# Optimization experiments

Measured on AMD Instinct MI355X. Metric: run time of the kernel, lower is better.

## Reference

```python
import jax, jax.numpy as jnp
import numpy as np

D_MODEL = 1024
N_HEADS = 16
D_HEAD = D_MODEL // N_HEADS
B, T = 4, 2048


def setup_inputs() -> dict:
    key = jax.random.key(0)
    k1, k2, k3 = jax.random.split(key, 3)
    x = jax.random.normal(k1, (B, T, D_MODEL), dtype=jnp.float32)
    # match nn.Linear init scale roughly (uniform ~ 1/sqrt(fan_in)); scale normal for stability
    w_qkv = jax.random.normal(k2, (D_MODEL, 3 * D_MODEL), dtype=jnp.float32) / np.sqrt(D_MODEL)
    w_out = jax.random.normal(k3, (D_MODEL, D_MODEL), dtype=jnp.float32) / np.sqrt(D_MODEL)
    return {"x": x, "w_qkv": w_qkv, "w_out": w_out}


def reference(x, w_qkv, w_out):
    Bx, Tx, D = x.shape
    H, Dh = N_HEADS, D_HEAD
    qkv = x @ w_qkv                                  # [B,T,3D]
    qkv = qkv.reshape(Bx, Tx, 3, H, Dh)
    q, k, v = qkv[:, :, 0], qkv[:, :, 1], qkv[:, :, 2]  # [B,T,H,Dh]
    scores = jnp.einsum('bqhd,bkhd->bhqk', q, k) / np.sqrt(Dh).astype(np.float32)
    mask = jnp.triu(jnp.ones((Tx, Tx), dtype=bool), k=1)  # causal: mask future
    scores = jnp.where(mask, -jnp.inf, scores)
    attn = jax.nn.softmax(scores, axis=-1)
    out = jnp.einsum('bhqk,bkhd->bqhd', attn, v).reshape(Bx, Tx, D)
    return out @ w_out
```

## Files before the change

kernel.cpp:

```cpp
#include <hip/hip_runtime.h>
#include <math.h>

#define T_SEQ 2048
#define NB 4
#define NH 16
#define DH 64
#define DM 1024

typedef __attribute__((ext_vector_type(8))) __bf16 bf16x8;
typedef __attribute__((ext_vector_type(4))) float f32x4;

typedef const __attribute__((address_space(1))) void* gas_t;
typedef __attribute__((address_space(3))) void* las_t;

__device__ inline bool detect_f32(const unsigned short* probe, int lane) {
    unsigned short u = probe[lane];
    int e = (u >> 7) & 0xFF;
    bool outlier = (e >= 140) || (e <= 90 && (u & 0x7fff) != 0);
    unsigned long long m = __ballot(outlier);
    return __popcll(m) >= 4;
}

__device__ inline bf16x8 load8_flex(const void* base, long elem, bool f32) {
    if (!f32) {
        return *(const bf16x8*)((const __bf16*)base + elem);
    } else {
        const float* f = (const float*)base + elem;
        float4 a = *(const float4*)f;
        float4 b = *(const float4*)(f + 4);
        bf16x8 r;
        r[0] = (__bf16)a.x; r[1] = (__bf16)a.y; r[2] = (__bf16)a.z; r[3] = (__bf16)a.w;
        r[4] = (__bf16)b.x; r[5] = (__bf16)b.y; r[6] = (__bf16)b.z; r[7] = (__bf16)b.w;
        return r;
    }
}

__global__ __launch_bounds__(256)
void cvt_x(const float* __restrict__ in, __bf16* __restrict__ out, long n8) {
    long i = (long)blockIdx.x * blockDim.x + threadIdx.x;
    if (i >= n8) return;
    const float* f = in + i * 8;
    float4 a = *(const float4*)f;
    float4 b = *(const float4*)(f + 4);
    bf16x8 r;
    r[0] = (__bf16)a.x; r[1] = (__bf16)a.y; r[2] = (__bf16)a.z; r[3] = (__bf16)a.w;
    r[4] = (__bf16)b.x; r[5] = (__bf16)b.y; r[6] = (__bf16)b.z; r[7] = (__bf16)b.w;
    *(bf16x8*)(out + i * 8) = r;
}

__global__ __launch_bounds__(256)
void tpose_cvt(const float* __restrict__ in, __bf16* __restrict__ out, int R, int C) {
    __shared__ __bf16 tile[32][33];
    const int bx = blockIdx.x * 32;
    const int by = blockIdx.y * 32;
    const int tx = threadIdx.x & 31;
    const int ty = threadIdx.x >> 5;
#pragma unroll
    for (int it = 0; it < 4; ++it) {
        int r = ty + it * 8;
        tile[r][tx] = (__bf16)in[(long)(by + r) * C + bx + tx];
    }
    __syncthreads();
#pragma unroll
    for (int it = 0; it < 4; ++it) {
        int r = ty + it * 8;
        out[(long)(bx + r) * R + by + tx] = tile[tx][r];
    }
}

__global__ __launch_bounds__(256)
void gemm_bt(const __bf16* __restrict__ A, long lda,
             const __bf16* __restrict__ Bt, long ldb,
             void* __restrict__ C, long ldc, int c_f32, int K) {
    __shared__ __align__(16) __bf16 sA[128 * 32];
    __shared__ __align__(16) __bf16 sB[128 * 32];
    const int tid  = threadIdx.x;
    const int lane = tid & 63;
    const int wave = tid >> 6;
    const int l15  = lane & 15;
    const int quad = lane >> 4;
    const int bm = blockIdx.y * 128;
    const int bn = blockIdx.x * 128;
    const int wm = (wave & 1) * 64;
    const int wn = (wave >> 1) * 64;

    f32x4 zero = {0.f, 0.f, 0.f, 0.f};
    f32x4 acc[4][4];
#pragma unroll
    for (int i = 0; i < 4; ++i)
#pragma unroll
        for (int j = 0; j < 4; ++j) acc[i][j] = zero;

    const int srow = tid >> 2;
    const int scol = (tid & 3) * 8;
    const __bf16* gA0 = A  + (long)(bm + srow) * lda + scol;
    const __bf16* gA1 = A  + (long)(bm + 64 + srow) * lda + scol;
    const __bf16* gB0 = Bt + (long)(bn + srow) * ldb + scol;
    const __bf16* gB1 = Bt + (long)(bn + 64 + srow) * ldb + scol;

    __bf16* lA0 = sA + wave * 512;
    __bf16* lA1 = sA + 2048 + wave * 512;
    __bf16* lB0 = sB + wave * 512;
    __bf16* lB1 = sB + 2048 + wave * 512;

    for (int k0 = 0; k0 < K; k0 += 32) {
        __syncthreads();
        __builtin_amdgcn_global_load_lds((gas_t)(gA0 + k0), (las_t)lA0, 16, 0, 0);
        __builtin_amdgcn_global_load_lds((gas_t)(gA1 + k0), (las_t)lA1, 16, 0, 0);
        __builtin_amdgcn_global_load_lds((gas_t)(gB0 + k0), (las_t)lB0, 16, 0, 0);
        __builtin_amdgcn_global_load_lds((gas_t)(gB1 + k0), (las_t)lB1, 16, 0, 0);
        __syncthreads();

        bf16x8 af[4], bfm[4];
#pragma unroll
        for (int i = 0; i < 4; ++i)
            af[i] = *(const bf16x8*)(sA + (wm + i * 16 + l15) * 32 + quad * 8);
#pragma unroll
        for (int j = 0; j < 4; ++j)
            bfm[j] = *(const bf16x8*)(sB + (wn + j * 16 + l15) * 32 + quad * 8);
#pragma unroll
        for (int i = 0; i < 4; ++i)
#pragma unroll
            for (int j = 0; j < 4; ++j)
                acc[i][j] = __builtin_amdgcn_mfma_f32_16x16x32_bf16(af[i], bfm[j], acc[i][j], 0, 0, 0);
    }

#pragma unroll
    for (int i = 0; i < 4; ++i)
#pragma unroll
        for (int j = 0; j < 4; ++j)
#pragma unroll
            for (int r = 0; r < 4; ++r) {
                int row = bm + wm + i * 16 + quad * 4 + r;
                int col = bn + wn + j * 16 + l15;
                if (c_f32)
                    ((float*)C)[(long)row * ldc + col] = acc[i][j][r];
                else
                    ((__bf16*)C)[(long)row * ldc + col] = (__bf16)acc[i][j][r];
            }
}

__global__ __launch_bounds__(256)
void gemm_bn(const void* __restrict__ A, long lda, long a0, int a_flex,
             const void* __restrict__ B, long ldb, int b_flex,
             void* __restrict__ C, long ldc, int c_flex, int K,
             const unsigned short* __restrict__ probe) {
    __shared__ __align__(16) __bf16 sA[128 * 32];
    __shared__ __align__(16) __bf16 sB[128 * 32];
    const int tid  = threadIdx.x;
    const int lane = tid & 63;
    const int wave = tid >> 6;
    const int l15  = lane & 15;
    const int quad = lane >> 4;
    const int bm = blockIdx.y * 128;
    const int bn = blockIdx.x * 128;
    const int wm = (wave & 1) * 64;
    const int wn = (wave >> 1) * 64;

    const bool is_f32 = detect_f32(probe, lane);
    const bool a_f32 = a_flex && is_f32;
    const bool b_f32 = b_flex && is_f32;
    const bool c_f32 = c_flex && is_f32;

    f32x4 zero = {0.f, 0.f, 0.f, 0.f};
    f32x4 acc[4][4];
#pragma unroll
    for (int i = 0; i < 4; ++i)
#pragma unroll
        for (int j = 0; j < 4; ++j) acc[i][j] = zero;

    const int srow = tid >> 2;
    const int scol = (tid & 3) * 8;

    for (int k0 = 0; k0 < K; k0 += 32) {
        __syncthreads();
        *(bf16x8*)(sA + tid * 8) =
            load8_flex(A, a0 + (long)(bm + srow) * lda + k0 + scol, a_f32);
        *(bf16x8*)(sA + 2048 + tid * 8) =
            load8_flex(A, a0 + (long)(bm + 64 + srow) * lda + k0 + scol, a_f32);
#pragma unroll
        for (int it = 0; it < 2; ++it) {
            int idx = tid + it * 256;
            int kk  = idx & 31;
            int n8  = (idx >> 5) * 8;
            bf16x8 bv = load8_flex(B, (long)(k0 + kk) * ldb + bn + n8, b_f32);
#pragma unroll
            for (int jj = 0; jj < 8; ++jj) sB[(n8 + jj) * 32 + kk] = bv[jj];
        }
        __syncthreads();

        bf16x8 af[4], bfm[4];
#pragma unroll
        for (int i = 0; i < 4; ++i)
            af[i] = *(const bf16x8*)(sA + (wm + i * 16 + l15) * 32 + quad * 8);
#pragma unroll
        for (int j = 0; j < 4; ++j)
            bfm[j] = *(const bf16x8*)(sB + (wn + j * 16 + l15) * 32 + quad * 8);
#pragma unroll
        for (int i = 0; i < 4; ++i)
#pragma unroll
            for (int j = 0; j < 4; ++j)
                acc[i][j] = __builtin_amdgcn_mfma_f32_16x16x32_bf16(af[i], bfm[j], acc[i][j], 0, 0, 0);
    }

#pragma unroll
    for (int i = 0; i < 4; ++i)
#pragma unroll
        for (int j = 0; j < 4; ++j)
#pragma unroll
            for (int r = 0; r < 4; ++r) {
                int row = bm + wm + i * 16 + quad * 4 + r;
                int col = bn + wn + j * 16 + l15;
                if (c_f32)
                    ((float*)C)[(long)row * ldc + col] = acc[i][j][r];
                else
                    ((__bf16*)C)[(long)row * ldc + col] = (__bf16)acc[i][j][r];
            }
}

__global__ __launch_bounds__(256)
void attn_k(__bf16* __restrict__ qkvp, int bhbits) {
    const int bid  = blockIdx.x;
    const int qt   = bid >> bhbits;
    const int bh   = bid & ((1 << bhbits) - 1);
    const int h    = bh & 15;
    const int b    = bh >> 4;
    const int tid  = threadIdx.x;
    const int lane = tid & 63;
    const int wave = tid >> 6;
    const int l15  = lane & 15;
    const int quad = lane >> 4;

    __shared__ __align__(16) __bf16 sK[64 * 72];
    __shared__ __align__(16) __bf16 sVT[64 * 64];
    __shared__ __align__(16) __bf16 sP[4][32 * 64];

    const long rs = 3 * DM;
    __bf16* base = qkvp + (long)b * T_SEQ * rs + h * DH;

    const int sr  = tid >> 3;
    const int sm  = tid & 7;
    const int sc8 = sm * 8;
    const int rot = 8 * ((5 * sm) & 7);
    const int vc0 = (sr + rot) & 63;
    const int vc1 = (sr + 32 + rot) & 63;

    const int q0  = qt * 128;
    const int wq0 = q0 + wave * 32;

    bf16x8 qa[2][2];
#pragma unroll
    for (int i = 0; i < 2; ++i)
#pragma unroll
        for (int kk = 0; kk < 2; ++kk) {
            bf16x8 v = *(const bf16x8*)(base + (long)(wq0 + i * 16 + l15) * rs + kk * 32 + quad * 8);
#pragma unroll
            for (int jj = 0; jj < 8; ++jj) v[jj] = (__bf16)((float)v[jj] * 0.125f);
            qa[i][kk] = v;
        }

    f32x4 zero = {0.f, 0.f, 0.f, 0.f};
    f32x4 o[2][4], o4[2];
#pragma unroll
    for (int i = 0; i < 2; ++i) {
        o4[i] = zero;
#pragma unroll
        for (int j = 0; j < 4; ++j) o[i][j] = zero;
    }

    bf16x8 vone;
#pragma unroll
    for (int jj = 0; jj < 8; ++jj) vone[jj] = (__bf16)1.0f;

    const int nk = (q0 + 128) >> 6;

    bf16x8 kreg[2], vreg[2];
#pragma unroll
    for (int it = 0; it < 2; ++it) {
        const __bf16* rp = base + (long)(sr + it * 32) * rs;
        kreg[it] = *(const bf16x8*)(rp + DM + sc8);
        vreg[it] = *(const bf16x8*)(rp + 2 * DM + sc8);
    }

    for (int t = 0; t < nk; ++t) {
        const int k0 = t * 64;
        __syncthreads();
        *(bf16x8*)(sK + sr * 72 + sc8)        = kreg[0];
        *(bf16x8*)(sK + (sr + 32) * 72 + sc8) = kreg[1];
#pragma unroll
        for (int jj = 0; jj < 8; ++jj) {
            sVT[(sc8 + jj) * 64 + vc0] = vreg[0][jj];
            sVT[(sc8 + jj) * 64 + vc1] = vreg[1][jj];
        }
        __syncthreads();

        if (t + 1 < nk) {
#pragma unroll
            for (int it = 0; it < 2; ++it) {
                const __bf16* rp = base + (long)(k0 + 64 + sr + it * 32) * rs;
                kreg[it] = *(const bf16x8*)(rp + DM + sc8);
                vreg[it] = *(const bf16x8*)(rp + 2 * DM + sc8);
            }
        }

        const bool active = (k0 <= wq0 + 31);
        if (active) {
            f32x4 s[2][4];
#pragma unroll
            for (int i = 0; i < 2; ++i)
#pragma unroll
                for (int j = 0; j < 4; ++j) s[i][j] = zero;
#pragma unroll
            for (int kk = 0; kk < 2; ++kk) {
                bf16x8 kb[4];
#pragma unroll
                for (int j = 0; j < 4; ++j)
                    kb[j] = *(const bf16x8*)(sK + (j * 16 + l15) * 72 + kk * 32 + quad * 8);
#pragma unroll
                for (int i = 0; i < 2; ++i)
#pragma unroll
                    for (int j = 0; j < 4; ++j)
                        s[i][j] = __builtin_amdgcn_mfma_f32_16x16x32_bf16(qa[i][kk], kb[j], s[i][j], 0, 0, 0);
            }

            const bool needmask = (k0 + 63 > wq0);
#pragma unroll
            for (int i = 0; i < 2; ++i)
#pragma unroll
                for (int r = 0; r < 4; ++r) {
                    const int qg = wq0 + i * 16 + quad * 4 + r;
#pragma unroll
                    for (int j = 0; j < 4; ++j) {
                        const int kg = k0 + j * 16 + l15;
                        float pv = __expf(fminf(s[i][j][r], 60.f));
                        if (needmask) pv = (kg > qg) ? 0.f : pv;
                        sP[wave][(i * 16 + quad * 4 + r) * 64 +
                                 ((j * 16 + l15 + 16 * quad) & 63)] = (__bf16)pv;
                    }
                }
        }

        __builtin_amdgcn_sched_barrier(0);
        __builtin_amdgcn_s_waitcnt(0xc07f);
        __builtin_amdgcn_sched_barrier(0);

        if (active) {
#pragma unroll
            for (int kk = 0; kk < 2; ++kk) {
                bf16x8 pa[2], vb[4];
#pragma unroll
                for (int i = 0; i < 2; ++i)
                    pa[i] = *(const bf16x8*)(
                        &sP[wave][(i * 16 + l15) * 64 +
                                  ((kk * 32 + quad * 8 + 16 * (l15 >> 2)) & 63)]);
#pragma unroll
                for (int j = 0; j < 4; ++j) {
                    const int g = (2 * j + (l15 >> 3)) & 7;
                    vb[j] = *(const bf16x8*)(
                        sVT + (j * 16 + l15) * 64 +
                        ((kk * 32 + quad * 8 + 8 * ((5 * g) & 7)) & 63));
                }
#pragma unroll
                for (int i = 0; i < 2; ++i) {
#pragma unroll
                    for (int j = 0; j < 4; ++j)
                        o[i][j] = __builtin_amdgcn_mfma_f32_16x16x32_bf16(pa[i], vb[j], o[i][j], 0, 0, 0);
                    o4[i] = __builtin_amdgcn_mfma_f32_16x16x32_bf16(pa[i], vone, o4[i], 0, 0, 0);
                }
            }
        }
    }

#pragma unroll
    for (int i = 0; i < 2; ++i)
#pragma unroll
        for (int r = 0; r < 4; ++r) {
            const int qg  = wq0 + i * 16 + quad * 4 + r;
            const float inv = 1.f / o4[i][r];
#pragma unroll
            for (int j = 0; j < 4; ++j)
                base[(long)qg * rs + j * 16 + l15] = (__bf16)(o[i][j][r] * inv);
        }
}

__global__ __launch_bounds__(256)
void fallback_k(float* __restrict__ out, long n, float wsmb) {
    long i = (long)blockIdx.x * blockDim.x + threadIdx.x;
    for (; i < n; i += (long)gridDim.x * blockDim.x) out[i] = 0.f;
    if (blockIdx.x == 0 && threadIdx.x == 0) out[0] = wsmb;
}

extern "C" void kernel_launch(void* const* d_in, const int* in_sizes, int n_in,
                              void* d_out, int out_size, void* d_ws, size_t ws_size,
                              hipStream_t stream) {
    const void* x     = d_in[0];
    const void* w_qkv = d_in[1];
    const void* w_out = d_in[2];
    const unsigned short* probe = (const unsigned short*)d_in[0];

    __bf16* qkv = (__bf16*)d_ws;
    __bf16* xb  = qkv + (size_t)8192 * 3072;
    __bf16* wtq = xb  + (size_t)8192 * 1024;
    __bf16* wto = wtq + (size_t)3072 * 1024;

    const size_t NEED_T1   = (size_t)72 * 1024 * 1024;
    const size_t NEED_FULL = (size_t)8192 * 3072 * 2;
    const size_t NEED_B    = (size_t)2048 * 3072 * 2;

    if (ws_size >= NEED_T1) {
        cvt_x<<<dim3(4096), 256, 0, stream>>>((const float*)x, xb, (long)8192 * 1024 / 8);
        tpose_cvt<<<dim3(96, 32), 256, 0, stream>>>((const float*)w_qkv, wtq, 1024, 3072);
        tpose_cvt<<<dim3(32, 32), 256, 0, stream>>>((const float*)w_out, wto, 1024, 1024);
        gemm_bt<<<dim3(24, 64), 256, 0, stream>>>(xb, 1024, wtq, 1024, qkv, 3072, 0, 1024);
        attn_k<<<dim3(16 * 64), 256, 0, stream>>>(qkv, 6);
        gemm_bt<<<dim3(8, 64), 256, 0, stream>>>(qkv, 3072, wto, 1024, d_out, 1024, 1, 1024);
    } else if (ws_size >= NEED_FULL) {
        gemm_bn<<<dim3(24, 64), 256, 0, stream>>>(
            x, 1024, 0, 1, w_qkv, 3072, 1, qkv, 3072, 0, 1024, probe);
        attn_k<<<dim3(16 * 64), 256, 0, stream>>>(qkv, 6);
        gemm_bn<<<dim3(8, 64), 256, 0, stream>>>(
            qkv, 3072, 0, 0, w_out, 1024, 1, d_out, 1024, 1, 1024, probe);
    } else if (ws_size >= NEED_B) {
        for (int b = 0; b < NB; ++b) {
            long xoff = (long)b * T_SEQ * DM;
            gemm_bn<<<dim3(24, 16), 256, 0, stream>>>(
                x, 1024, xoff, 1, w_qkv, 3072, 1, qkv, 3072, 0, 1024, probe);
            attn_k<<<dim3(16 * 16), 256, 0, stream>>>(qkv, 4);
            gemm_bn<<<dim3(8, 16), 256, 0, stream>>>(
                qkv, 3072, 0, 0, w_out, 1024, 1,
                (void*)((char*)d_out + (size_t)b * T_SEQ * DM * 4),
                1024, 1, 1024, probe);
        }
    } else {
        fallback_k<<<dim3(512), 256, 0, stream>>>(
            (float*)d_out, (long)8192 * 1024, (float)(ws_size >> 20));
    }
}
```

Baseline: 307.7 us.

## Pair causal query tiles per block and use 8 waves of 16 rows

The attention kernel now launches 512-thread blocks with 8 waves, each wave owning 16 query rows instead of 32. Each block processes two query tiles (p and 15-p) in sequence, which balances the causal workload across blocks and halves the grid. Each K/V tile staged into shared memory is shared by more waves, and fewer registers are needed per wave. The cost is less MFMA reuse of each K/V fragment per wave and a serialized second pass inside every block.

```diff
diff --git a/kernel.cpp b/kernel.cpp
--- a/kernel.cpp
+++ b/kernel.cpp
@@ -218,10 +218,10 @@
             }
 }
 
-__global__ __launch_bounds__(256)
+__global__ __launch_bounds__(512, 4)
 void attn_k(__bf16* __restrict__ qkvp, int bhbits) {
     const int bid  = blockIdx.x;
-    const int qt   = bid >> bhbits;
+    const int p    = bid >> bhbits;
     const int bh   = bid & ((1 << bhbits) - 1);
     const int h    = bh & 15;
     const int b    = bh >> 4;
@@ -233,7 +233,7 @@
 
     __shared__ __align__(16) __bf16 sK[64 * 72];
     __shared__ __align__(16) __bf16 sVT[64 * 64];
-    __shared__ __align__(16) __bf16 sP[4][32 * 64];
+    __shared__ __align__(16) __bf16 sP[8][16 * 64];
 
     const long rs = 3 * DM;
     __bf16* base = qkvp + (long)b * T_SEQ * rs + h * DH;
@@ -242,145 +242,123 @@
     const int sm  = tid & 7;
     const int sc8 = sm * 8;
     const int rot = 8 * ((5 * sm) & 7);
-    const int vc0 = (sr + rot) & 63;
-    const int vc1 = (sr + 32 + rot) & 63;
-
-    const int q0  = qt * 128;
-    const int wq0 = q0 + wave * 32;
-
-    bf16x8 qa[2][2];
-#pragma unroll
-    for (int i = 0; i < 2; ++i)
+    const int vcol = (sr + rot) & 63;
+
+    bf16x8 vone;
+#pragma unroll
+    for (int jj = 0; jj < 8; ++jj) vone[jj] = (__bf16)1.0f;
+
+    f32x4 zero = {0.f, 0.f, 0.f, 0.f};
+
+#pragma unroll 1
+    for (int half = 0; half < 2; ++half) {
+        const int qt  = half ? (15 - p) : p;
+        const int q0  = qt * 128;
+        const int wq0 = q0 + wave * 16;
+        const int nk  = (q0 + 128) >> 6;
+
+        bf16x8 qa[2];
 #pragma unroll
         for (int kk = 0; kk < 2; ++kk) {
-            bf16x8 v = *(const bf16x8*)(base + (long)(wq0 + i * 16 + l15) * rs + kk * 32 + quad * 8);
+            bf16x8 v = *(const bf16x8*)(base + (long)(wq0 + l15) * rs + kk * 32 + quad * 8);
 #pragma unroll
             for (int jj = 0; jj < 8; ++jj) v[jj] = (__bf16)((float)v[jj] * 0.125f);
-            qa[i][kk] = v;
-        }
-
-    f32x4 zero = {0.f, 0.f, 0.f, 0.f};
-    f32x4 o[2][4], o4[2];
-#pragma unroll
-    for (int i = 0; i < 2; ++i) {
-        o4[i] = zero;
-#pragma unroll
-        for (int j = 0; j < 4; ++j) o[i][j] = zero;
-    }
-
-    bf16x8 vone;
-#pragma unroll
-    for (int jj = 0; jj < 8; ++jj) vone[jj] = (__bf16)1.0f;
-
-    const int nk = (q0 + 128) >> 6;
-
-    bf16x8 kreg[2], vreg[2];
-#pragma unroll
-    for (int it = 0; it < 2; ++it) {
-        const __bf16* rp = base + (long)(sr + it * 32) * rs;
-        kreg[it] = *(const bf16x8*)(rp + DM + sc8);
-        vreg[it] = *(const bf16x8*)(rp + 2 * DM + sc8);
-    }
-
-    for (int t = 0; t < nk; ++t) {
-        const int k0 = t * 64;
-        __syncthreads();
-        *(bf16x8*)(sK + sr * 72 + sc8)        = kreg[0];
-        *(bf16x8*)(sK + (sr + 32) * 72 + sc8) = kreg[1];
-#pragma unroll
-        for (int jj = 0; jj < 8; ++jj) {
-            sVT[(sc8 + jj) * 64 + vc0] = vreg[0][jj];
-            sVT[(sc8 + jj) * 64 + vc1] = vreg[1][jj];
-        }
-        __syncthreads();
-
-        if (t + 1 < nk) {
-#pragma unroll
-            for (int it = 0; it < 2; ++it) {
-                const __bf16* rp = base + (long)(k0 + 64 + sr + it * 32) * rs;
-                kreg[it] = *(const bf16x8*)(rp + DM + sc8);
-                vreg[it] = *(const bf16x8*)(rp + 2 * DM + sc8);
+            qa[kk] = v;
+        }
+
+        f32x4 o[4], o4;
+        o4 = zero;
+#pragma unroll
+        for (int j = 0; j < 4; ++j) o[j] = zero;
+
+        bf16x8 kreg, vreg;
+        {
+            const __bf16* rp = base + (long)sr * rs;
+            kreg = *(const bf16x8*)(rp + DM + sc8);
+            vreg = *(const bf16x8*)(rp + 2 * DM + sc8);
+        }
+
+        for (int t = 0; t < nk; ++t) {
+            const int k0 = t * 64;
+            __syncthreads();
+            *(bf16x8*)(sK + sr * 72 + sc8) = kreg;
+#pragma unroll
+            for (int jj = 0; jj < 8; ++jj)
+                sVT[(sc8 + jj) * 64 + vcol] = vreg[jj];
+            __syncthreads();
+
+            if (t + 1 < nk) {
+                const __bf16* rp = base + (long)(k0 + 64 + sr) * rs;
+                kreg = *(const bf16x8*)(rp + DM + sc8);
+                vreg = *(const bf16x8*)(rp + 2 * DM + sc8);
             }
-        }
-
-        const bool active = (k0 <= wq0 + 31);
-        if (active) {
-            f32x4 s[2][4];
-#pragma unroll
-            for (int i = 0; i < 2; ++i)
-#pragma unroll
-                for (int j = 0; j < 4; ++j) s[i][j] = zero;
-#pragma unroll
-            for (int kk = 0; kk < 2; ++kk) {
-                bf16x8 kb[4];
-#pragma unroll
-                for (int j = 0; j < 4; ++j)
-                    kb[j] = *(const bf16x8*)(sK + (j * 16 + l15) * 72 + kk * 32 + quad * 8);
-#pragma unroll
-                for (int i = 0; i < 2; ++i)
+
+            const bool active = (k0 <= wq0 + 15);
+            if (active) {
+                f32x4 s[4];
+#pragma unroll
+                for (int j = 0; j < 4; ++j) s[j] = zero;
+#pragma unroll
+                for (int kk = 0; kk < 2; ++kk) {
+                    bf16x8 kb[4];
 #pragma unroll
                     for (int j = 0; j < 4; ++j)
-                        s[i][j] = __builtin_amdgcn_mfma_f32_16x16x32_bf16(qa[i][kk], kb[j], s[i][j], 0, 0, 0);
-            }
-
-            const bool needmask = (k0 + 63 > wq0);
-#pragma unroll
-            for (int i = 0; i < 2; ++i)
+                        kb[j] = *(const bf16x8*)(sK + (j * 16 + l15) * 72 + kk * 32 + quad * 8);
+#pragma unroll
+                    for (int j = 0; j < 4; ++j)
+                        s[j] = __builtin_amdgcn_mfma_f32_16x16x32_bf16(qa[kk], kb[j], s[j], 0, 0, 0);
+                }
+
+                const bool needmask = (k0 + 63 > wq0);
 #pragma unroll
                 for (int r = 0; r < 4; ++r) {
-                    const int qg = wq0 + i * 16 + quad * 4 + r;
+                    const int qg = wq0 + quad * 4 + r;
 #pragma unroll
                     for (int j = 0; j < 4; ++j) {
                         const int kg = k0 + j * 16 + l15;
-                        float pv = __expf(fminf(s[i][j][r], 60.f));
+                        float pv = __expf(fminf(s[j][r], 60.f));
                         if (needmask) pv = (kg > qg) ? 0.f : pv;
-                        sP[wave][(i * 16 + quad * 4 + r) * 64 +
+                        sP[wave][(quad * 4 + r) * 64 +
                                  ((j * 16 + l15 + 16 * quad) & 63)] = (__bf16)pv;
                     }
                 }
-        }
-
-        __builtin_amdgcn_sched_barrier(0);
-        __builtin_amdgcn_s_waitcnt(0xc07f);
-        __builtin_amdgcn_sched_barrier(0);
-
-        if (active) {
-#pragma unroll
-            for (int kk = 0; kk < 2; ++kk) {
-                bf16x8 pa[2], vb[4];
-#pragma unroll
-                for (int i = 0; i < 2; ++i)
-                    pa[i] = *(const bf16x8*)(
-                        &sP[wave][(i * 16 + l15) * 64 +
+            }
+
+            __builtin_amdgcn_sched_barrier(0);
+            __builtin_amdgcn_s_waitcnt(0xc07f);
+            __builtin_amdgcn_sched_barrier(0);
+
+            if (active) {
+#pragma unroll
+                for (int kk = 0; kk < 2; ++kk) {
+                    bf16x8 pa, vb[4];
+                    pa = *(const bf16x8*)(
+                        &sP[wave][l15 * 64 +
                                   ((kk * 32 + quad * 8 + 16 * (l15 >> 2)) & 63)]);
 #pragma unroll
-                for (int j = 0; j < 4; ++j) {
-                    const int g = (2 * j + (l15 >> 3)) & 7;
-                    vb[j] = *(const bf16x8*)(
-                        sVT + (j * 16 + l15) * 64 +
-                        ((kk * 32 + quad * 8 + 8 * ((5 * g) & 7)) & 63));
-                }
-#pragma unroll
-                for (int i = 0; i < 2; ++i) {
+                    for (int j = 0; j < 4; ++j) {
+                        const int g = (2 * j + (l15 >> 3)) & 7;
+                        vb[j] = *(const bf16x8*)(
+                            sVT + (j * 16 + l15) * 64 +
+                            ((kk * 32 + quad * 8 + 8 * ((5 * g) & 7)) & 63));
+                    }
 #pragma unroll
                     for (int j = 0; j < 4; ++j)
-                        o[i][j] = __builtin_amdgcn_mfma_f32_16x16x32_bf16(pa[i], vb[j], o[i][j], 0, 0, 0);
-                    o4[i] = __builtin_amdgcn_mfma_f32_16x16x32_bf16(pa[i], vone, o4[i], 0, 0, 0);
+                        o[j] = __builtin_amdgcn_mfma_f32_16x16x32_bf16(pa, vb[j], o[j], 0, 0, 0);
+                    o4 = __builtin_amdgcn_mfma_f32_16x16x32_bf16(pa, vone, o4, 0, 0, 0);
                 }
             }
         }
-    }
-
-#pragma unroll
-    for (int i = 0; i < 2; ++i)
+
 #pragma unroll
         for (int r = 0; r < 4; ++r) {
-            const int qg  = wq0 + i * 16 + quad * 4 + r;
-            const float inv = 1.f / o4[i][r];
+            const int qg  = wq0 + quad * 4 + r;
+            const float inv = 1.f / o4[r];
 #pragma unroll
             for (int j = 0; j < 4; ++j)
-                base[(long)qg * rs + j * 16 + l15] = (__bf16)(o[i][j][r] * inv);
-        }
+                base[(long)qg * rs + j * 16 + l15] = (__bf16)(o[j][r] * inv);
+        }
+    }
 }
 
 __global__ __launch_bounds__(256)
@@ -412,12 +390,12 @@
         tpose_cvt<<<dim3(96, 32), 256, 0, stream>>>((const float*)w_qkv, wtq, 1024, 3072);
         tpose_cvt<<<dim3(32, 32), 256, 0, stream>>>((const float*)w_out, wto, 1024, 1024);
         gemm_bt<<<dim3(24, 64), 256, 0, stream>>>(xb, 1024, wtq, 1024, qkv, 3072, 0, 1024);
-        attn_k<<<dim3(16 * 64), 256, 0, stream>>>(qkv, 6);
+        attn_k<<<dim3(8 * 64), 512, 0, stream>>>(qkv, 6);
         gemm_bt<<<dim3(8, 64), 256, 0, stream>>>(qkv, 3072, wto, 1024, d_out, 1024, 1, 1024);
     } else if (ws_size >= NEED_FULL) {
         gemm_bn<<<dim3(24, 64), 256, 0, stream>>>(
             x, 1024, 0, 1, w_qkv, 3072, 1, qkv, 3072, 0, 1024, probe);
-        attn_k<<<dim3(16 * 64), 256, 0, stream>>>(qkv, 6);
+        attn_k<<<dim3(8 * 64), 512, 0, stream>>>(qkv, 6);
         gemm_bn<<<dim3(8, 64), 256, 0, stream>>>(
             qkv, 3072, 0, 0, w_out, 1024, 1, d_out, 1024, 1, 1024, probe);
     } else if (ws_size >= NEED_B) {
@@ -425,7 +403,7 @@
             long xoff = (long)b * T_SEQ * DM;
             gemm_bn<<<dim3(24, 16), 256, 0, stream>>>(
                 x, 1024, xoff, 1, w_qkv, 3072, 1, qkv, 3072, 0, 1024, probe);
-            attn_k<<<dim3(16 * 16), 256, 0, stream>>>(qkv, 4);
+            attn_k<<<dim3(8 * 16), 512, 0, stream>>>(qkv, 4);
             gemm_bn<<<dim3(8, 16), 256, 0, stream>>>(
                 qkv, 3072, 0, 0, w_out, 1024, 1,
                 (void*)((char*)d_out + (size_t)b * T_SEQ * DM * 4),
```

Measured after the change: 282.6 us. -8.2%, faster.
